# Kernel optimization log

Measured on AMD Instinct MI355X. Metric: run time of the kernel, lower is better.

## Reference

```python
import jax, jax.numpy as jnp
import numpy as np

DEPTH = 4
EPS = 1e-5


def _bn(x, g, b):
    # training-mode BatchNorm over (B,H,W) per channel
    m = x.mean(axis=(0, 2, 3), keepdims=True)
    v = x.var(axis=(0, 2, 3), keepdims=True)
    return (x - m) * jax.lax.rsqrt(v + EPS) * g[None, :, None, None] + b[None, :, None, None]


def _conv_bn(x, w, g, b):
    # 1x1 conv (no bias) + BatchNorm
    y = jnp.einsum('bchw,oc->bohw', x, w)
    return _bn(y, g, b)


def _block_max_broadcast(x, gsz):
    # max over each (H/gsz, W/gsz) block of a gsz x gsz grid, broadcast back
    B, C, H, W = x.shape
    xr = x.reshape(B, C, gsz, H // gsz, gsz, W // gsz)
    m = xr.max(axis=(3, 5), keepdims=True)
    return jnp.broadcast_to(m, xr.shape).reshape(B, C, H, W)


def setup_inputs() -> dict:
    key = jax.random.key(0)
    ks = jax.random.split(key, 3)
    B, C, H, W = 4, 128, 256, 256
    x = jax.random.normal(ks[0], (B, C, H, W), dtype=jnp.float32)
    conv_w = jax.random.normal(ks[1], (DEPTH, C, C), dtype=jnp.float32) * 0.05
    conv_g = jnp.ones((DEPTH, C), dtype=jnp.float32)
    conv_b = jnp.zeros((DEPTH, C), dtype=jnp.float32)
    final_w = jax.random.normal(ks[2], (C, (DEPTH + 1) * C), dtype=jnp.float32) * 0.05
    final_g = jnp.ones((C,), dtype=jnp.float32)
    final_b = jnp.zeros((C,), dtype=jnp.float32)
    return {"x": x, "conv_w": conv_w, "conv_g": conv_g, "conv_b": conv_b,
            "final_w": final_w, "final_g": final_g, "final_b": final_b}


def reference(x, conv_w, conv_g, conv_b, final_w, final_g, final_b):
    # p[0]: identity; p[1+d]: block-max over 2^d x 2^d grid broadcast back, then 1x1 conv+BN
    p = [x]
    for d in range(DEPTH):
        pooled = _block_max_broadcast(x, 2 ** d)  # d=0 -> global max broadcast
        p.append(_conv_bn(pooled, conv_w[d], conv_g[d], conv_b[d]))
    out = jnp.concatenate(p, axis=1)  # [B, 5C, H, W]
    return _conv_bn(out, final_w, final_g, final_b)
```

## Files before the change

### kernel.cpp

```cpp
#include <hip/hip_runtime.h>
#include <hip/hip_bf16.h>
#include <math.h>
#include <float.h>

#define B_ 4
#define C_ 128
#define P_ 65536

#define M3_OFF      0
#define M2_OFF      32768
#define M1_OFF      40960
#define M0_OFF      43008
#define YBASE_      43520
#define SCALED_OFF  87040
#define SHIFTD_OFF  87552
#define CONTRIB_OFF 88064
#define S3_OFF      120832
#define SX_OFF      153600
#define G_OFF       154112
#define SCALEF_OFF  219648
#define SHIFTF_OFF  219776
#define MAXP_OFF    219904
#define SUMP_OFF    744192

using short8 = __attribute__((ext_vector_type(8))) short;
using f32x4 = __attribute__((ext_vector_type(4))) float;
using f32x16 = __attribute__((ext_vector_type(16))) float;

__device__ __forceinline__ int level_rel(int d) {
    return YBASE_ - 512 * (((1 << (2 * (d + 1))) - 1) / 3);
}

__device__ __forceinline__ unsigned int bfpair(float a, float b) {
    unsigned int ua = __float_as_uint(a), ub = __float_as_uint(b);
    ua = (ua + 0x7fffu + ((ua >> 16) & 1u)) >> 16;
    ub = (ub + 0x7fffu + ((ub >> 16) & 1u)) & 0xffff0000u;
    return ua | ub;
}

#define GLDS16(src, dst)                                                    \
    __builtin_amdgcn_global_load_lds(                                       \
        (const __attribute__((address_space(1))) unsigned int*)(src),       \
        (__attribute__((address_space(3))) unsigned int*)(dst), 16, 0, 0)

__global__ __launch_bounds__(256) void k_gram_pool(const float* __restrict__ x,
                                                   float* __restrict__ ws,
                                                   float* __restrict__ gpart) {
    __shared__ float buf[4][4096];
    int wg = blockIdx.x;
    int b = wg >> 7, rc = wg & 127;
    const float* xb = x + (size_t)b * C_ * P_ + (size_t)rc * 512;
    int t_ = threadIdx.x, l = t_ & 63, wv = t_ >> 6;
    int tr = (wv >> 1) * 64;
    int tcc = (wv & 1) * 64;
    bool doacc = ((wv & 1) == 0);
    int lrow = l >> 3, lch = l & 7;

    f32x16 acc[2][2];
#pragma unroll
    for (int i = 0; i < 2; ++i)
#pragma unroll
        for (int j = 0; j < 2; ++j)
#pragma unroll
            for (int r = 0; r < 16; ++r) acc[i][j][r] = 0.f;
    float mxA[2][8], smA[2][8];
#pragma unroll
    for (int i = 0; i < 2; ++i)
#pragma unroll
        for (int j = 0; j < 8; ++j) { mxA[i][j] = -FLT_MAX; smA[i][j] = 0.f; }

#define ISSUE(tt)                                                            \
    do {                                                                     \
        _Pragma("unroll") for (int i_ = 0; i_ < 4; ++i_) {                   \
            int row_ = wv * 32 + i_ * 8 + lrow;                              \
            int ch_ = lch ^ (row_ & 7);                                      \
            GLDS16(xb + (size_t)row_ * P_ + (tt) * 32 + ch_ * 4,             \
                   &buf[(tt) & 3][(wv * 32 + i_ * 8) * 32]);                 \
        }                                                                    \
    } while (0)

    ISSUE(0);
    ISSUE(1);
    ISSUE(2);

#pragma unroll
    for (int t = 0; t < 16; ++t) {
        if (t <= 13)
            asm volatile("s_waitcnt vmcnt(8)" ::: "memory");
        else if (t == 14)
            asm volatile("s_waitcnt vmcnt(4)" ::: "memory");
        else
            asm volatile("s_waitcnt vmcnt(0)" ::: "memory");
        __builtin_amdgcn_sched_barrier(0);
        __builtin_amdgcn_s_barrier();
        asm volatile("" ::: "memory");
        __builtin_amdgcn_sched_barrier(0);
        if (t + 3 < 16) ISSUE(t + 3);

        const float* tl = &buf[t & 3][0];
        int jc = t & 7;
#pragma unroll
        for (int ks = 0; ks < 2; ++ks) {
            int ch = ks * 4 + ((l >> 5) << 1);
            short8 fr[4];
#pragma unroll
            for (int fi = 0; fi < 4; ++fi) {
                int row = (fi < 2 ? tr : tcc) + (fi & 1) * 32 + (l & 31);
                int sw = row & 7;
                const float* p0 = tl + row * 32 + ((ch ^ sw) << 2);
                const float* p1 = tl + row * 32 + (((ch + 1) ^ sw) << 2);
                float4 v0 = *(const float4*)p0;
                float4 v1 = *(const float4*)p1;
                if (fi < 2 && doacc) {
                    mxA[fi][jc] = fmaxf(mxA[fi][jc],
                        fmaxf(fmaxf(fmaxf(v0.x, v0.y), fmaxf(v0.z, v0.w)),
                              fmaxf(fmaxf(v1.x, v1.y), fmaxf(v1.z, v1.w))));
                    smA[fi][jc] += ((v0.x + v0.y) + (v0.z + v0.w)) +
                                   ((v1.x + v1.y) + (v1.z + v1.w));
                }
                union { uint4 u; short8 s8; } cu;
                cu.u = make_uint4(bfpair(v0.x, v0.y), bfpair(v0.z, v0.w),
                                  bfpair(v1.x, v1.y), bfpair(v1.z, v1.w));
                fr[fi] = cu.s8;
            }
            acc[0][0] = __builtin_amdgcn_mfma_f32_32x32x16_bf16(fr[0], fr[2], acc[0][0], 0, 0, 0);
            acc[0][1] = __builtin_amdgcn_mfma_f32_32x32x16_bf16(fr[0], fr[3], acc[0][1], 0, 0, 0);
            acc[1][0] = __builtin_amdgcn_mfma_f32_32x32x16_bf16(fr[1], fr[2], acc[1][0], 0, 0, 0);
            acc[1][1] = __builtin_amdgcn_mfma_f32_32x32x16_bf16(fr[1], fr[3], acc[1][1], 0, 0, 0);
        }
    }
#undef ISSUE

    size_t gb = (size_t)wg * 16384;
#pragma unroll
    for (int i = 0; i < 2; ++i)
#pragma unroll
        for (int j = 0; j < 2; ++j)
#pragma unroll
            for (int r = 0; r < 16; ++r) {
                int row = tr + i * 32 + (r & 3) + 8 * (r >> 2) + 4 * (l >> 5);
                int col = tcc + j * 32 + (l & 31);
                gpart[gb + (size_t)row * 128 + col] = acc[i][j][r];
            }
    if (doacc) {
        int i3 = rc >> 4, rr = rc & 15;
#pragma unroll
        for (int half = 0; half < 2; ++half)
#pragma unroll
            for (int jc = 0; jc < 8; ++jc) {
                float m = mxA[half][jc], sv = smA[half][jc];
                m = fmaxf(m, __shfl_xor(m, 32));
                sv += __shfl_xor(sv, 32);
                if (l < 32) {
                    int c = tr + half * 32 + l;
                    size_t idx = ((size_t)(b * 128 + c) * 64 + i3 * 8 + jc) * 16 + rr;
                    ws[MAXP_OFF + idx] = m;
                    ws[SUMP_OFF + idx] = sv;
                }
            }
    }
}

__global__ __launch_bounds__(256) void k_reduceG(const float* __restrict__ gpart,
                                                 float* __restrict__ ws) {
    int tid = blockIdx.x * 256 + threadIdx.x;
    int b = tid >> 14, inner = tid & 16383;
    const float* p = gpart + (size_t)b * 128 * 16384 + inner;
    float s = 0.f;
    for (int r = 0; r < 128; ++r) s += p[(size_t)r * 16384];
    ws[G_OFF + tid] = s;
}

__global__ __launch_bounds__(256) void k_reduceMS(float* __restrict__ ws) {
    int bc = blockIdx.x;
    int t = threadIdx.x;
    int blk = t >> 2, q = t & 3;
    __shared__ float bm[64], bs[64];
    __shared__ float lv[24];
    __shared__ float sxr[8];
    {
        size_t base = (size_t)bc * 1024 + blk * 16 + q * 4;
        float4 mv = *(const float4*)(ws + MAXP_OFF + base);
        float4 sv = *(const float4*)(ws + SUMP_OFF + base);
        float m = fmaxf(fmaxf(mv.x, mv.y), fmaxf(mv.z, mv.w));
        float s = (sv.x + sv.y) + (sv.z + sv.w);
        m = fmaxf(m, __shfl_xor(m, 1)); s += __shfl_xor(s, 1);
        m = fmaxf(m, __shfl_xor(m, 2)); s += __shfl_xor(s, 2);
        if (q == 0) {
            bm[blk] = m;
            bs[blk] = s;
            ws[M3_OFF + (size_t)bc * 64 + blk] = m;
            ws[S3_OFF + (size_t)bc * 64 + blk] = s;
        }
    }
    __syncthreads();
    if (t < 8) {
        float sx = 0.f;
        for (int r = 0; r < 8; ++r) sx += bs[t * 8 + r];
        sxr[t] = sx;
    }
    if (t < 16) {
        int i2 = t >> 2, j2 = t & 3;
        float m = -FLT_MAX;
        for (int a = 0; a < 2; ++a)
            for (int b2 = 0; b2 < 2; ++b2)
                m = fmaxf(m, bm[(2 * i2 + a) * 8 + 2 * j2 + b2]);
        lv[t] = m;
        ws[M2_OFF + (size_t)bc * 16 + t] = m;
    }
    __syncthreads();
    if (t == 0) {
        float sx = 0.f;
        for (int r = 0; r < 8; ++r) sx += sxr[r];
        ws[SX_OFF + bc] = sx;
    }
    if (t < 4) {
        int i1 = t >> 1, j1 = t & 1;
        float m = -FLT_MAX;
        for (int a = 0; a < 2; ++a)
            for (int b2 = 0; b2 < 2; ++b2)
                m = fmaxf(m, lv[(2 * i1 + a) * 4 + 2 * j1 + b2]);
        lv[16 + t] = m;
        ws[M1_OFF + (size_t)bc * 4 + t] = m;
    }
    __syncthreads();
    if (t == 0)
        ws[M0_OFF + bc] = fmaxf(fmaxf(lv[16], lv[17]), fmaxf(lv[18], lv[19]));
}

__global__ __launch_bounds__(256) void k_conv_pool(const float* __restrict__ conv_w,
                                                   float* __restrict__ ws) {
    int bid = blockIdx.x;
    int d = bid >> 4, b = (bid >> 2) & 3, cchunk = bid & 3;
    int NB = 1 << (2 * d);
    int rel = level_rel(d);
    const float* Mb = ws + rel + (size_t)b * 128 * NB;
    float* Yb = ws + YBASE_ + rel + (size_t)b * 128 * NB;
    __shared__ float mlds[8192];
    int t = threadIdx.x;
    int tot = 128 * NB;
    for (int i = t; i < tot; i += 256) mlds[i] = Mb[i];
    __syncthreads();
    if (NB >= 4) {
        int nbq = NB >> 2;
        int nq = 32 * nbq;
        for (int qi = t; qi < nq; qi += 256) {
            int co = cchunk * 32 + (qi >> (2 * d - 2));
            int bq = qi & (nbq - 1);
            const float* wrow = conv_w + ((size_t)d * 128 + co) * 128;
            float a0 = 0.f, a1 = 0.f, a2 = 0.f, a3 = 0.f;
            for (int ci = 0; ci < 128; ++ci) {
                float4 mv = *(const float4*)(&mlds[ci * NB + bq * 4]);
                float wvv = wrow[ci];
                a0 = fmaf(wvv, mv.x, a0);
                a1 = fmaf(wvv, mv.y, a1);
                a2 = fmaf(wvv, mv.z, a2);
                a3 = fmaf(wvv, mv.w, a3);
            }
            float4 r;
            r.x = a0; r.y = a1; r.z = a2; r.w = a3;
            *(float4*)(&Yb[co * NB + bq * 4]) = r;
        }
    } else {
        for (int oi = t; oi < 32; oi += 256) {
            int co = cchunk * 32 + oi;
            const float* wrow = conv_w + (size_t)co * 128;
            float acc = 0.f;
            for (int ci = 0; ci < 128; ++ci) acc = fmaf(mlds[ci], wrow[ci], acc);
            Yb[co] = acc;
        }
    }
}

__global__ __launch_bounds__(256) void k_bnstats_d(const float* __restrict__ conv_g,
                                                   const float* __restrict__ conv_b,
                                                   float* __restrict__ ws) {
    int tid = blockIdx.x * 256 + threadIdx.x;
    if (tid >= 512) return;
    int d = tid >> 7, c = tid & 127;
    int NB = 1 << (2 * d);
    const float* Y = ws + YBASE_ + level_rel(d);
    int n = 4 * NB;
    float s = 0.f;
    for (int b = 0; b < 4; ++b)
        for (int k = 0; k < NB; ++k) s += Y[((size_t)b * 128 + c) * NB + k];
    float mean = s / (float)n;
    float v = 0.f;
    for (int b = 0; b < 4; ++b)
        for (int k = 0; k < NB; ++k) {
            float dd = Y[((size_t)b * 128 + c) * NB + k] - mean;
            v = fmaf(dd, dd, v);
        }
    float var = v / (float)n;
    float sc = conv_g[d * 128 + c] * rsqrtf(var + 1e-5f);
    ws[SCALED_OFF + tid] = sc;
    ws[SHIFTD_OFF + tid] = conv_b[d * 128 + c] - mean * sc;
}

__global__ __launch_bounds__(128) void k_contrib(const float* __restrict__ final_w,
                                                 float* __restrict__ ws) {
    int b = blockIdx.x >> 6, blk3 = blockIdx.x & 63;
    int i3 = blk3 >> 3, j3 = blk3 & 7;
    __shared__ float pn[512];
    int t = threadIdx.x;
    for (int k = t; k < 512; k += 128) {
        int d = k >> 7, c = k & 127;
        int sh = 3 - d;
        int blkd = (i3 >> sh) * (1 << d) + (j3 >> sh);
        int NB = 1 << (2 * d);
        float yv = ws[YBASE_ + level_rel(d) + ((size_t)b * 128 + c) * NB + blkd];
        pn[k] = yv * ws[SCALED_OFF + k] + ws[SHIFTD_OFF + k];
    }
    __syncthreads();
    const float* fw = final_w + (size_t)t * 640 + 128;
    float acc = 0.f;
#pragma unroll 8
    for (int k = 0; k < 512; k += 4) {
        float4 f = *(const float4*)(fw + k);
        acc = fmaf(pn[k], f.x, acc);
        acc = fmaf(pn[k + 1], f.y, acc);
        acc = fmaf(pn[k + 2], f.z, acc);
        acc = fmaf(pn[k + 3], f.w, acc);
    }
    ws[CONTRIB_OFF + ((size_t)b * 128 + t) * 64 + blk3] = acc;
}

__global__ __launch_bounds__(128) void k_stats(const float* __restrict__ final_w,
                                               const float* __restrict__ final_g,
                                               const float* __restrict__ final_b,
                                               float* __restrict__ ws) {
    int o = blockIdx.x, t = threadIdx.x;
    __shared__ __align__(16) float wlds[128];
    __shared__ __align__(16) float cvl[64];
    __shared__ float rbuf[4];
    wlds[t] = final_w[(size_t)o * 640 + t];
    __syncthreads();
    float SSQ = 0.f, SUM = 0.f;
    for (int b = 0; b < 4; ++b) {
        if (t < 64) cvl[t] = ws[CONTRIB_OFF + (size_t)(b * 128 + o) * 64 + t];
        __syncthreads();
        const float* Gb = ws + G_OFF + (size_t)b * 16384 + (size_t)t * 128;
        float a1 = 0.f;
#pragma unroll 8
        for (int k = 0; k < 128; k += 4) {
            float4 g = *(const float4*)(Gb + k);
            float4 w = *(const float4*)(&wlds[k]);
            a1 = fmaf(g.x, w.x, fmaf(g.y, w.y, fmaf(g.z, w.z, fmaf(g.w, w.w, a1))));
        }
        const float* S3p = ws + S3_OFF + (size_t)(b * 128 + t) * 64;
        float a2 = 0.f;
#pragma unroll 8
        for (int k = 0; k < 64; k += 4) {
            float4 sv = *(const float4*)(S3p + k);
            float4 cv = *(const float4*)(&cvl[k]);
            a2 = fmaf(sv.x, cv.x, fmaf(sv.y, cv.y, fmaf(sv.z, cv.z, fmaf(sv.w, cv.w, a2))));
        }
        float r1 = (a1 + 2.f * a2) * wlds[t];
        float r2 = wlds[t] * ws[SX_OFF + b * 128 + t];
        if (t < 64) {
            r1 += 1024.f * cvl[t] * cvl[t];
            r2 += 1024.f * cvl[t];
        }
#pragma unroll
        for (int k = 1; k < 64; k <<= 1) {
            r1 += __shfl_xor(r1, k);
            r2 += __shfl_xor(r2, k);
        }
        if ((t & 63) == 0) {
            rbuf[(t >> 6) * 2] = r1;
            rbuf[(t >> 6) * 2 + 1] = r2;
        }
        __syncthreads();
        SSQ += rbuf[0] + rbuf[2];
        SUM += rbuf[1] + rbuf[3];
        __syncthreads();
    }
    if (t == 0) {
        float mean = SUM / 262144.f;
        float var = SSQ / 262144.f - mean * mean;
        float sc = final_g[o] * rsqrtf(var + 1e-5f);
        ws[SCALEF_OFF + o] = sc;
        ws[SHIFTF_OFF + o] = final_b[o] - mean * sc;
    }
}

__global__ __launch_bounds__(256) void k_out(const float* __restrict__ x,
                                             const float* __restrict__ final_w,
                                             const float* __restrict__ ws,
                                             float* __restrict__ out) {
    __shared__ uint4 wtileq[2048];
    __shared__ float scl[128], shf[128], cvs[512];
    unsigned char* wtile = (unsigned char*)wtileq;
    int wgid = blockIdx.x;
    int b = wgid >> 9, pt = wgid & 511;
    int p0 = pt * 128;
    int t = threadIdx.x, l = t & 63, wv = t >> 6;
#pragma unroll
    for (int it = 0; it < 32; ++it) {
        int pid = it * 256 + t;
        int o = pid >> 6, cp = (pid & 63) * 2;
        float2 f = *(const float2*)(final_w + (size_t)o * 640 + cp);
        unsigned int u = bfpair(f.x, f.y);
        int wa = (o * 256 + cp * 2) ^ ((o & 7) << 4);
        *(unsigned int*)(wtile + wa) = u;
    }
    if (t < 128) {
        scl[t] = ws[SCALEF_OFF + t];
        shf[t] = ws[SHIFTF_OFF + t];
    }
    int i3 = pt >> 6, jb = (pt & 1) * 4;
    for (int q = t; q < 512; q += 256) {
        int o = q >> 2, jj = q & 3;
        cvs[q] = ws[CONTRIB_OFF + (size_t)(b * 128 + o) * 64 + i3 * 8 + jb + jj];
    }
    __syncthreads();

    const float* xb = x + (size_t)b * C_ * P_;
    int pw = p0 + wv * 32;
    f32x4 acc[8][2];
#pragma unroll
    for (int i = 0; i < 8; ++i) {
        acc[i][0] = (f32x4){0.f, 0.f, 0.f, 0.f};
        acc[i][1] = (f32x4){0.f, 0.f, 0.f, 0.f};
    }
#pragma unroll
    for (int ks = 0; ks < 4; ++ks) {
        short8 bf[2];
#pragma unroll
        for (int nt = 0; nt < 2; ++nt) {
            const float* xp = xb + (size_t)(ks * 32 + (l >> 4) * 8) * P_ + (pw + nt * 16 + (l & 15));
            float f0 = xp[0 * P_], f1 = xp[1 * P_], f2 = xp[2 * P_], f3 = xp[3 * P_];
            float f4 = xp[4 * P_], f5 = xp[5 * P_], f6 = xp[6 * P_], f7 = xp[7 * P_];
            union { uint4 u; short8 s; } cvtu;
            cvtu.u = make_uint4(bfpair(f0, f1), bfpair(f2, f3), bfpair(f4, f5), bfpair(f6, f7));
            bf[nt] = cvtu.s;
        }
#pragma unroll
        for (int mt = 0; mt < 8; ++mt) {
            int ra = ((mt * 16 + (l & 15)) * 256 + ks * 64 + (l >> 4) * 16) ^ ((l & 7) << 4);
            short8 af = *(const short8*)(wtile + ra);
            acc[mt][0] = __builtin_amdgcn_mfma_f32_16x16x32_bf16(af, bf[0], acc[mt][0], 0, 0, 0);
            acc[mt][1] = __builtin_amdgcn_mfma_f32_16x16x32_bf16(af, bf[1], acc[mt][1], 0, 0, 0);
        }
    }
#pragma unroll
    for (int mt = 0; mt < 8; ++mt)
#pragma unroll
        for (int nt = 0; nt < 2; ++nt) {
            int p = pw + nt * 16 + (l & 15);
            int jj = ((p & 255) >> 5) & 3;
#pragma unroll
            for (int r = 0; r < 4; ++r) {
                int o = mt * 16 + (l >> 4) * 4 + r;
                float z = acc[mt][nt][r] + cvs[o * 4 + jj];
                out[(size_t)(b * 128 + o) * P_ + p] = fmaf(z, scl[o], shf[o]);
            }
        }
}

extern "C" void kernel_launch(void* const* d_in, const int* in_sizes, int n_in,
                              void* d_out, int out_size, void* d_ws, size_t ws_size,
                              hipStream_t stream) {
    const float* x = (const float*)d_in[0];
    const float* conv_w = (const float*)d_in[1];
    const float* conv_g = (const float*)d_in[2];
    const float* conv_b = (const float*)d_in[3];
    const float* final_w = (const float*)d_in[4];
    const float* final_g = (const float*)d_in[5];
    const float* final_b = (const float*)d_in[6];
    float* out = (float*)d_out;
    float* ws = (float*)d_ws;

    k_gram_pool<<<512, 256, 0, stream>>>(x, ws, out);
    k_reduceG<<<256, 256, 0, stream>>>(out, ws);
    k_reduceMS<<<512, 256, 0, stream>>>(ws);
    k_conv_pool<<<64, 256, 0, stream>>>(conv_w, ws);
    k_bnstats_d<<<2, 256, 0, stream>>>(conv_g, conv_b, ws);
    k_contrib<<<B_ * 64, 128, 0, stream>>>(final_w, ws);
    k_stats<<<128, 128, 0, stream>>>(final_w, final_g, final_b, ws);
    k_out<<<2048, 256, 0, stream>>>(x, final_w, ws, out);
}
```

Baseline: 196.1 us.

## Split gram tile across eight waves and use hardware bf16 pair conversion

The Gram/pool kernel now runs 512 threads per block. Each of 8 waves owns one 32-row strip and two 32-column tiles, where before 4 waves each owned 64x64. Each wave issues half as many async LDS loads, with wait counts adjusted to match. Manual bf16 rounding is replaced by the HIP float2-to-bfloat162 intrinsic. The intent is more latency hiding from extra waves and fewer registers per wave, at the cost of more LDS fragment reads overall (B-fragments are no longer shared across as many MFMAs) and more barrier participants.

Result: no change. 194.0 us (-1.1%).

```diff
diff --git a/kernel.cpp b/kernel.cpp
--- a/kernel.cpp
+++ b/kernel.cpp
@@ -32,10 +32,9 @@
 }
 
 __device__ __forceinline__ unsigned int bfpair(float a, float b) {
-    unsigned int ua = __float_as_uint(a), ub = __float_as_uint(b);
-    ua = (ua + 0x7fffu + ((ua >> 16) & 1u)) >> 16;
-    ub = (ub + 0x7fffu + ((ub >> 16) & 1u)) & 0xffff0000u;
-    return ua | ub;
+    union { __hip_bfloat162 h2; unsigned int u; } cv;
+    cv.h2 = __float22bfloat162_rn(make_float2(a, b));
+    return cv.u;
 }
 
 #define GLDS16(src, dst)                                                    \
@@ -43,39 +42,35 @@
         (const __attribute__((address_space(1))) unsigned int*)(src),       \
         (__attribute__((address_space(3))) unsigned int*)(dst), 16, 0, 0)
 
-__global__ __launch_bounds__(256) void k_gram_pool(const float* __restrict__ x,
-                                                   float* __restrict__ ws,
-                                                   float* __restrict__ gpart) {
+__global__ __launch_bounds__(512, 4) void k_gram_pool(const float* __restrict__ x,
+                                                      float* __restrict__ ws,
+                                                      float* __restrict__ gpart) {
     __shared__ float buf[4][4096];
     int wg = blockIdx.x;
     int b = wg >> 7, rc = wg & 127;
     const float* xb = x + (size_t)b * C_ * P_ + (size_t)rc * 512;
     int t_ = threadIdx.x, l = t_ & 63, wv = t_ >> 6;
-    int tr = (wv >> 1) * 64;
-    int tcc = (wv & 1) * 64;
-    bool doacc = ((wv & 1) == 0);
+    int qi = wv & 3;
+    int qjb = (wv >> 2) * 2;
+    bool doacc = (wv < 4);
     int lrow = l >> 3, lch = l & 7;
 
-    f32x16 acc[2][2];
-#pragma unroll
-    for (int i = 0; i < 2; ++i)
-#pragma unroll
-        for (int j = 0; j < 2; ++j)
-#pragma unroll
-            for (int r = 0; r < 16; ++r) acc[i][j][r] = 0.f;
-    float mxA[2][8], smA[2][8];
-#pragma unroll
-    for (int i = 0; i < 2; ++i)
-#pragma unroll
-        for (int j = 0; j < 8; ++j) { mxA[i][j] = -FLT_MAX; smA[i][j] = 0.f; }
+    f32x16 acc[2];
+#pragma unroll
+    for (int j = 0; j < 2; ++j)
+#pragma unroll
+        for (int r = 0; r < 16; ++r) acc[j][r] = 0.f;
+    float mxA[8], smA[8];
+#pragma unroll
+    for (int j = 0; j < 8; ++j) { mxA[j] = -FLT_MAX; smA[j] = 0.f; }
 
 #define ISSUE(tt)                                                            \
     do {                                                                     \
-        _Pragma("unroll") for (int i_ = 0; i_ < 4; ++i_) {                   \
-            int row_ = wv * 32 + i_ * 8 + lrow;                              \
+        _Pragma("unroll") for (int i_ = 0; i_ < 2; ++i_) {                   \
+            int row_ = wv * 16 + i_ * 8 + lrow;                              \
             int ch_ = lch ^ (row_ & 7);                                      \
             GLDS16(xb + (size_t)row_ * P_ + (tt) * 32 + ch_ * 4,             \
-                   &buf[(tt) & 3][(wv * 32 + i_ * 8) * 32]);                 \
+                   &buf[(tt) & 3][(wv * 16 + i_ * 8) * 32]);                 \
         }                                                                    \
     } while (0)
 
@@ -86,9 +81,9 @@
 #pragma unroll
     for (int t = 0; t < 16; ++t) {
         if (t <= 13)
-            asm volatile("s_waitcnt vmcnt(8)" ::: "memory");
+            asm volatile("s_waitcnt vmcnt(4)" ::: "memory");
         else if (t == 14)
-            asm volatile("s_waitcnt vmcnt(4)" ::: "memory");
+            asm volatile("s_waitcnt vmcnt(2)" ::: "memory");
         else
             asm volatile("s_waitcnt vmcnt(0)" ::: "memory");
         __builtin_amdgcn_sched_barrier(0);
@@ -102,62 +97,62 @@
 #pragma unroll
         for (int ks = 0; ks < 2; ++ks) {
             int ch = ks * 4 + ((l >> 5) << 1);
-            short8 fr[4];
-#pragma unroll
-            for (int fi = 0; fi < 4; ++fi) {
-                int row = (fi < 2 ? tr : tcc) + (fi & 1) * 32 + (l & 31);
+            short8 fa;
+            {
+                int row = qi * 32 + (l & 31);
                 int sw = row & 7;
-                const float* p0 = tl + row * 32 + ((ch ^ sw) << 2);
-                const float* p1 = tl + row * 32 + (((ch + 1) ^ sw) << 2);
-                float4 v0 = *(const float4*)p0;
-                float4 v1 = *(const float4*)p1;
-                if (fi < 2 && doacc) {
-                    mxA[fi][jc] = fmaxf(mxA[fi][jc],
+                float4 v0 = *(const float4*)(tl + row * 32 + ((ch ^ sw) << 2));
+                float4 v1 = *(const float4*)(tl + row * 32 + (((ch + 1) ^ sw) << 2));
+                if (doacc) {
+                    mxA[jc] = fmaxf(mxA[jc],
                         fmaxf(fmaxf(fmaxf(v0.x, v0.y), fmaxf(v0.z, v0.w)),
                               fmaxf(fmaxf(v1.x, v1.y), fmaxf(v1.z, v1.w))));
-                    smA[fi][jc] += ((v0.x + v0.y) + (v0.z + v0.w)) +
-                                   ((v1.x + v1.y) + (v1.z + v1.w));
+                    smA[jc] += ((v0.x + v0.y) + (v0.z + v0.w)) +
+                               ((v1.x + v1.y) + (v1.z + v1.w));
                 }
                 union { uint4 u; short8 s8; } cu;
                 cu.u = make_uint4(bfpair(v0.x, v0.y), bfpair(v0.z, v0.w),
                                   bfpair(v1.x, v1.y), bfpair(v1.z, v1.w));
-                fr[fi] = cu.s8;
+                fa = cu.s8;
             }
-            acc[0][0] = __builtin_amdgcn_mfma_f32_32x32x16_bf16(fr[0], fr[2], acc[0][0], 0, 0, 0);
-            acc[0][1] = __builtin_amdgcn_mfma_f32_32x32x16_bf16(fr[0], fr[3], acc[0][1], 0, 0, 0);
-            acc[1][0] = __builtin_amdgcn_mfma_f32_32x32x16_bf16(fr[1], fr[2], acc[1][0], 0, 0, 0);
-            acc[1][1] = __builtin_amdgcn_mfma_f32_32x32x16_bf16(fr[1], fr[3], acc[1][1], 0, 0, 0);
+#pragma unroll
+            for (int j = 0; j < 2; ++j) {
+                int row = (qjb + j) * 32 + (l & 31);
+                int sw = row & 7;
+                float4 v0 = *(const float4*)(tl + row * 32 + ((ch ^ sw) << 2));
+                float4 v1 = *(const float4*)(tl + row * 32 + (((ch + 1) ^ sw) << 2));
+                union { uint4 u; short8 s8; } cu;
+                cu.u = make_uint4(bfpair(v0.x, v0.y), bfpair(v0.z, v0.w),
+                                  bfpair(v1.x, v1.y), bfpair(v1.z, v1.w));
+                acc[j] = __builtin_amdgcn_mfma_f32_32x32x16_bf16(fa, cu.s8, acc[j], 0, 0, 0);
+            }
         }
     }
 #undef ISSUE
 
     size_t gb = (size_t)wg * 16384;
 #pragma unroll
-    for (int i = 0; i < 2; ++i)
-#pragma unroll
-        for (int j = 0; j < 2; ++j)
-#pragma unroll
-            for (int r = 0; r < 16; ++r) {
-                int row = tr + i * 32 + (r & 3) + 8 * (r >> 2) + 4 * (l >> 5);
-                int col = tcc + j * 32 + (l & 31);
-                gpart[gb + (size_t)row * 128 + col] = acc[i][j][r];
-            }
+    for (int j = 0; j < 2; ++j)
+#pragma unroll
+        for (int r = 0; r < 16; ++r) {
+            int row = qi * 32 + (r & 3) + 8 * (r >> 2) + 4 * (l >> 5);
+            int col = (qjb + j) * 32 + (l & 31);
+            gpart[gb + (size_t)row * 128 + col] = acc[j][r];
+        }
     if (doacc) {
         int i3 = rc >> 4, rr = rc & 15;
 #pragma unroll
-        for (int half = 0; half < 2; ++half)
-#pragma unroll
-            for (int jc = 0; jc < 8; ++jc) {
-                float m = mxA[half][jc], sv = smA[half][jc];
-                m = fmaxf(m, __shfl_xor(m, 32));
-                sv += __shfl_xor(sv, 32);
-                if (l < 32) {
-                    int c = tr + half * 32 + l;
-                    size_t idx = ((size_t)(b * 128 + c) * 64 + i3 * 8 + jc) * 16 + rr;
-                    ws[MAXP_OFF + idx] = m;
-                    ws[SUMP_OFF + idx] = sv;
-                }
+        for (int jc = 0; jc < 8; ++jc) {
+            float m = mxA[jc], sv = smA[jc];
+            m = fmaxf(m, __shfl_xor(m, 32));
+            sv += __shfl_xor(sv, 32);
+            if (l < 32) {
+                int c = qi * 32 + l;
+                size_t idx = ((size_t)(b * 128 + c) * 64 + i3 * 8 + jc) * 16 + rr;
+                ws[MAXP_OFF + idx] = m;
+                ws[SUMP_OFF + idx] = sv;
             }
+        }
     }
 }
 
@@ -471,7 +466,7 @@
     float* out = (float*)d_out;
     float* ws = (float*)d_ws;
 
-    k_gram_pool<<<512, 256, 0, stream>>>(x, ws, out);
+    k_gram_pool<<<512, 512, 0, stream>>>(x, ws, out);
     k_reduceG<<<256, 256, 0, stream>>>(out, ws);
     k_reduceMS<<<512, 256, 0, stream>>>(ws);
     k_conv_pool<<<64, 256, 0, stream>>>(conv_w, ws);
```
